# Kernel tuning notes

Measured on AMD Instinct MI355X. Metric: run time of the kernel, lower is better.

Reference implementation:

```python
import jax, jax.numpy as jnp
import numpy as np

B, L, D, H, PD = 4, 8192, 512, 8, 1
DK = D // H
EPS = 1e-5


def setup_inputs() -> dict:
    root = jax.random.key(0)
    ks = jax.random.split(root, 16)
    s = 0.02
    inp = {
        'query': jax.random.normal(ks[0], (B, L, D), jnp.float32),
        'key': jax.random.normal(ks[1], (B, L, D), jnp.float32),
        'value': jax.random.normal(ks[2], (B, L, D), jnp.float32),
        'pos': jax.random.uniform(ks[3], (B, L, PD), jnp.float32),
        # QKV projections (xavier-ish small + diagonal init, as in _reset_parameters)
        'Wq': s * jax.random.normal(ks[4], (D, D), jnp.float32) + 0.01 * jnp.eye(D),
        'bq': jnp.zeros((D,), jnp.float32),
        'Wk': s * jax.random.normal(ks[5], (D, D), jnp.float32) + 0.01 * jnp.eye(D),
        'bk': jnp.zeros((D,), jnp.float32),
        'Wv': s * jax.random.normal(ks[6], (D, D), jnp.float32) + 0.01 * jnp.eye(D),
        'bv': jnp.zeros((D,), jnp.float32),
        # per-head LayerNorm affine params for K and V: [H, DK]
        'gK': jnp.ones((H, DK), jnp.float32),
        'betaK': jnp.zeros((H, DK), jnp.float32),
        'gV': jnp.ones((H, DK), jnp.float32),
        'betaV': jnp.zeros((H, DK), jnp.float32),
        # output fc: (D + H*PD) -> D
        'fcW': s * jax.random.normal(ks[7], (D, D + H * PD), jnp.float32),
        'fcb': jnp.zeros((D,), jnp.float32),
    }
    return inp


def _proj(x, W, b):
    # [B,L,D] -> [B,H,L,DK]
    return (x @ W.T + b).reshape(B, L, H, DK).transpose(0, 2, 1, 3)


def _head_layernorm(x, g, b):
    # x: [B,H,L,DK]; per-head affine params g,b: [H,DK]; biased variance (torch LN)
    m = x.mean(-1, keepdims=True)
    v = x.var(-1, keepdims=True)
    xn = (x - m) * jax.lax.rsqrt(v + EPS)
    return xn * g[None, :, None, :] + b[None, :, None, :]


def reference(query, key, value, pos, Wq, bq, Wk, bk, Wv, bv,
              gK, betaK, gV, betaV, fcW, fcb):
    q = _proj(query, Wq, bq)
    k = _proj(key, Wk, bk)
    v = _proj(value, Wv, bv)
    k = _head_layernorm(k, gK, betaK)
    v = _head_layernorm(v, gV, betaV)
    # positional concat: pos [B,L,PD] -> [B,H,L,PD], concat on feature dim
    p = jnp.broadcast_to(pos[:, None, :, :], (B, H, L, PD))
    q = jnp.concatenate([p, q], axis=-1)  # [B,H,L,DK+PD]
    k = jnp.concatenate([p, k], axis=-1)
    v = jnp.concatenate([p, v], axis=-1)
    # Galerkin linear attention: (K^T V)/L then Q @ that
    attn = jnp.einsum('bhld,bhle->bhde', k, v) / L  # [B,H,DK+PD,DK+PD]
    out = jnp.einsum('bhld,bhde->bhle', q, attn)    # [B,H,L,DK+PD]
    out = out.transpose(0, 2, 1, 3).reshape(B, L, H * (DK + PD))
    att_output = out @ fcW.T + fcb  # [B,L,D]
    return (att_output, attn)
```

## Files before the change

kernel.cpp:

```cpp
#include <hip/hip_runtime.h>

typedef __attribute__((ext_vector_type(8))) short short8;
typedef __attribute__((ext_vector_type(4))) float f32x4;
typedef __attribute__((ext_vector_type(4))) unsigned short ushort4v;
typedef __attribute__((ext_vector_type(4))) unsigned int uint4v;
typedef unsigned short ushort;
typedef unsigned int uint;

#define B_  4
#define L_  8192
#define D_  512
#define H_  8
#define F_  65
#define CF_ 520
#define CFP_ 544
#define KVS_ 80
#define EPS_ 1e-5f

__device__ __forceinline__ ushort f2b(float f) {
    uint x = __float_as_uint(f);
    uint r = (x + 0x7FFFu + ((x >> 16) & 1u)) >> 16;
    return (ushort)r;
}
__device__ __forceinline__ float b2f(ushort u) {
    return __uint_as_float(((uint)u) << 16);
}

#define GLD16(gptr, sptr) \
    __builtin_amdgcn_global_load_lds((const __attribute__((address_space(1))) void*)(gptr), \
                                     (__attribute__((address_space(3))) void*)(sptr), 16, 0, 0)

__device__ __forceinline__ size_t pk_off(int col, int row) {
    return (size_t)(col >> 5) * 4096 + (size_t)(((col >> 3) & 3) * 1024 + row * 8 + (col & 7));
}

__global__ __launch_bounds__(256)
void cast_w(const float* __restrict__ Wq, const float* __restrict__ Wk,
            const float* __restrict__ Wv, ushort* __restrict__ Wb)
{
    const int g = blockIdx.x * 256 + threadIdx.x;
    const int inner = g & 511;
    const int tileIdx = g >> 9;
    const int w   = inner >> 7;
    const int row = inner & 127;
    const int ks  = tileIdx & 15;
    const int nt  = (tileIdx >> 4) & 3;
    const int z   = tileIdx >> 6;
    const float* __restrict__ src = (z == 0) ? Wq : (z == 1) ? Wk : Wv;
    const float* s = &src[(size_t)(nt * 128 + row) * D_ + ks * 32 + w * 8];
    const float4 f0 = *(const float4*)s;
    const float4 f1 = *(const float4*)(s + 4);
    short8 v;
    v[0] = (short)f2b(f0.x); v[1] = (short)f2b(f0.y);
    v[2] = (short)f2b(f0.z); v[3] = (short)f2b(f0.w);
    v[4] = (short)f2b(f1.x); v[5] = (short)f2b(f1.y);
    v[6] = (short)f2b(f1.z); v[7] = (short)f2b(f1.w);
    *(short8*)&Wb[(size_t)tileIdx * 4096 + inner * 8] = v;
}

__global__ __launch_bounds__(256, 2)
void proj_mfma(const float* __restrict__ Xq, const float* __restrict__ Xk,
               const float* __restrict__ Xv, const ushort* __restrict__ Wb,
               const float* __restrict__ bq, const float* __restrict__ bk,
               const float* __restrict__ bv, const float* __restrict__ pos,
               const float* __restrict__ gK, const float* __restrict__ betaK,
               const float* __restrict__ gV, const float* __restrict__ betaV,
               ushort* __restrict__ Qc, ushort* __restrict__ Kh,
               ushort* __restrict__ Vh)
{
    const int x  = blockIdx.x;
    const int m0 = (((x >> 4) << 3) + (x & 7)) * 128;
    const int nh = (x >> 3) & 1;
    const int n0 = nh * 256;
    const int z  = blockIdx.y;

    const float*  __restrict__ X    = (z == 0) ? Xq : (z == 1) ? Xk : Xv;
    const float*  __restrict__ bias = (z == 0) ? bq : (z == 1) ? bk : bv;

    const int t  = threadIdx.x;
    const int w  = t >> 6, l = t & 63;
    const int wm = (w >> 1) * 64, wn = (w & 1) * 128;
    const int lg = l >> 4, lm = l & 15;

    __shared__ __align__(16) float sAf[2][4096];
    __shared__ __align__(16) short sB[2][8192];

    f32x4 acc[4][8];
#pragma unroll
    for (int i = 0; i < 4; ++i)
#pragma unroll
        for (int j = 0; j < 8; ++j) acc[i][j] = (f32x4){0.f, 0.f, 0.f, 0.f};

    const int lr = l >> 3;
    const int hg = (l & 7) ^ lr;
    const float* ag[4]; int alo[4];
#pragma unroll
    for (int i = 0; i < 4; ++i) {
        const int row = (w * 4 + i) * 8 + lr;
        ag[i]  = &X[(size_t)(m0 + row) * D_ + hg * 4];
        alo[i] = (w * 4 + i) * 256;
    }

    const ushort* bsrc0 = Wb + (size_t)((z * 4 + nh * 2) * 16) * 4096 + w * 1024 + l * 8;
    const ushort* bsrc1 = bsrc0 + (size_t)16 * 4096;
    const int blo0 = w * 1024, blo1 = w * 1024 + 512;

    int a0o[4], a1o[4], bro[8];
#pragma unroll
    for (int i = 0; i < 4; ++i) {
        const int r = wm + i * 16 + lm;
        a0o[i] = r * 32 + (((lg * 2)     ^ (r & 7)) * 4);
        a1o[i] = r * 32 + (((lg * 2 + 1) ^ (r & 7)) * 4);
    }
#pragma unroll
    for (int i = 0; i < 8; ++i) {
        const int col = wn + i * 16 + lm;
        bro[i] = (col >> 7) * 4096 + lg * 1024 + (col & 127) * 8;
    }

    auto stage = [&](int ks, int buf) {
#pragma unroll
        for (int i = 0; i < 4; ++i) GLD16(ag[i] + ks * 32, &sAf[buf][alo[i]]);
        GLD16(bsrc0 + (size_t)ks * 4096,       &sB[buf][blo0]);
        GLD16(bsrc0 + (size_t)ks * 4096 + 512, &sB[buf][blo1]);
        GLD16(bsrc1 + (size_t)ks * 4096,       &sB[buf][4096 + blo0]);
        GLD16(bsrc1 + (size_t)ks * 4096 + 512, &sB[buf][4096 + blo1]);
    };

    stage(0, 0);
    int cur = 0;
#pragma unroll
    for (int ks = 0; ks < 16; ++ks) {
        __syncthreads();
        if (ks < 15) stage(ks + 1, cur ^ 1);

        short8 af[4], bfv[8];
#pragma unroll
        for (int i = 0; i < 4; ++i) {
            const f32x4 A0 = *(const f32x4*)&sAf[cur][a0o[i]];
            const f32x4 A1 = *(const f32x4*)&sAf[cur][a1o[i]];
            uint u0, u1, u2, u3;
            asm("v_cvt_pk_bf16_f32 %0, %1, %2" : "=v"(u0) : "v"(A0[0]), "v"(A0[1]));
            asm("v_cvt_pk_bf16_f32 %0, %1, %2" : "=v"(u1) : "v"(A0[2]), "v"(A0[3]));
            asm("v_cvt_pk_bf16_f32 %0, %1, %2" : "=v"(u2) : "v"(A1[0]), "v"(A1[1]));
            asm("v_cvt_pk_bf16_f32 %0, %1, %2" : "=v"(u3) : "v"(A1[2]), "v"(A1[3]));
            union { uint4v u4; short8 s8; } cv;
            cv.u4 = (uint4v){u0, u1, u2, u3};
            af[i] = cv.s8;
        }
#pragma unroll
        for (int i = 0; i < 8; ++i) bfv[i] = *(const short8*)&sB[cur][bro[i]];
#pragma unroll
        for (int mt = 0; mt < 4; ++mt)
#pragma unroll
            for (int nt = 0; nt < 8; ++nt)
                acc[mt][nt] = __builtin_amdgcn_mfma_f32_16x16x32_bf16(
                    af[mt], bfv[nt], acc[mt][nt], 0, 0, 0);

        cur ^= 1;
    }

    const int h0 = (n0 + wn) >> 6;
    float bvv[8];
#pragma unroll
    for (int nt = 0; nt < 8; ++nt) bvv[nt] = bias[n0 + wn + nt * 16 + lm];

    if (z == 0) {
#pragma unroll
        for (int mt = 0; mt < 4; ++mt) {
#pragma unroll
            for (int r = 0; r < 4; ++r) {
                const int m = m0 + wm + mt * 16 + lg * 4 + r;
                const int mtile = m >> 7, rowin = m & 127;
                ushort* tb = Qc + (size_t)(mtile * 17) * 4096 + rowin * 8;
#pragma unroll
                for (int nt = 0; nt < 8; ++nt) {
                    const int col = (h0 + (nt >> 2)) * F_ + 1 + (nt & 3) * 16 + lm;
                    tb[pk_off(col, 0)] = f2b(acc[mt][nt][r] + bvv[nt]);
                }
                if (lm == 15) {
                    tb[pk_off(h0 * F_, 0)]       = f2b(pos[m]);
                    tb[pk_off((h0 + 1) * F_, 0)] = f2b(pos[m]);
                }
                if (h0 == 6 && lm < 12) {
                    const int wreg = 1 + (lm >> 2);
                    const int e2 = (lm & 3) * 2;
                    *(uint*)&tb[(size_t)16 * 4096 + wreg * 1024 + e2] = 0u;
                }
            }
        }
    } else {
        const float* gp = (z == 1) ? gK : gV;
        const float* bp = (z == 1) ? betaK : betaV;
        ushort* Oh = (z == 1) ? Kh : Vh;
        float gg[8], bb2[8];
#pragma unroll
        for (int nt = 0; nt < 8; ++nt) {
            const int idx = (h0 + (nt >> 2)) * 64 + (nt & 3) * 16 + lm;
            gg[nt]  = gp[idx];
            bb2[nt] = bp[idx];
        }
#pragma unroll
        for (int mt = 0; mt < 4; ++mt) {
#pragma unroll
            for (int r = 0; r < 4; ++r) {
                const int m = m0 + wm + mt * 16 + lg * 4 + r;
                const int bb = m >> 13, ll = m & 8191;
#pragma unroll
                for (int g = 0; g < 2; ++g) {
                    const float v0 = acc[mt][g * 4 + 0][r] + bvv[g * 4 + 0];
                    const float v1 = acc[mt][g * 4 + 1][r] + bvv[g * 4 + 1];
                    const float v2 = acc[mt][g * 4 + 2][r] + bvv[g * 4 + 2];
                    const float v3 = acc[mt][g * 4 + 3][r] + bvv[g * 4 + 3];
                    float s = v0 + v1 + v2 + v3;
                    float q = v0 * v0 + v1 * v1 + v2 * v2 + v3 * v3;
                    s += __shfl_xor(s, 1); s += __shfl_xor(s, 2);
                    s += __shfl_xor(s, 4); s += __shfl_xor(s, 8);
                    q += __shfl_xor(q, 1); q += __shfl_xor(q, 2);
                    q += __shfl_xor(q, 4); q += __shfl_xor(q, 8);
                    const float mean = s * (1.f / 64.f);
                    const float var = q * (1.f / 64.f) - mean * mean;
                    const float rs = rsqrtf(var + EPS_);
                    const int h = h0 + g;
                    ushort* row = Oh + ((size_t)(bb * H_ + h) * L_ + ll) * KVS_;
                    row[1 + 0 * 16 + lm] = f2b((v0 - mean) * rs * gg[g * 4 + 0] + bb2[g * 4 + 0]);
                    row[1 + 1 * 16 + lm] = f2b((v1 - mean) * rs * gg[g * 4 + 1] + bb2[g * 4 + 1]);
                    row[1 + 2 * 16 + lm] = f2b((v2 - mean) * rs * gg[g * 4 + 2] + bb2[g * 4 + 2]);
                    row[1 + 3 * 16 + lm] = f2b((v3 - mean) * rs * gg[g * 4 + 3] + bb2[g * 4 + 3]);
                    if (lm == 15) row[0] = f2b(pos[m]);
                    else          row[F_ + lm] = 0;
                }
            }
        }
    }
}

__global__ __launch_bounds__(256)
void attn_accum(const ushort* __restrict__ Kh, const ushort* __restrict__ Vh,
                float* __restrict__ attn_acc)
{
    const int s = blockIdx.x;
    const int h = blockIdx.y;
    const int b = blockIdx.z;
    const int t = threadIdx.x;

    __shared__ __align__(16) float Ks[64][84];
    __shared__ __align__(16) float Vs[64][84];

    const size_t base = ((size_t)(b * H_ + h) * L_ + s * 512) * KVS_;

    float acc[5][5];
#pragma unroll
    for (int i = 0; i < 5; ++i)
#pragma unroll
        for (int j = 0; j < 5; ++j) acc[i][j] = 0.f;

    const int dg = t / 13, eg = t % 13;
    const bool act = (t < 169);
    const int d0 = dg * 5, e0 = eg * 5;

    for (int c = 0; c < 8; ++c) {
#pragma unroll
        for (int i = 0; i < 3; ++i) {
            const int slot = t + i * 256;
            if (slot < 640) {
                const int r = slot / 10;
                const int cc = (slot - r * 10) * 8;
                const size_t g = base + (size_t)(c * 64 + r) * KVS_ + cc;
                const short8 kv = *(const short8*)(const void*)&Kh[g];
                const short8 vv = *(const short8*)(const void*)&Vh[g];
                float* kd = &Ks[r][cc];
                float* vd = &Vs[r][cc];
#pragma unroll
                for (int e = 0; e < 8; ++e) {
                    kd[e] = b2f((ushort)kv[e]);
                    vd[e] = b2f((ushort)vv[e]);
                }
            }
        }
        __syncthreads();
        if (act) {
#pragma unroll 2
            for (int l = 0; l < 64; ++l) {
                float kf[5], vf[5];
#pragma unroll
                for (int i = 0; i < 5; ++i) kf[i] = Ks[l][d0 + i];
#pragma unroll
                for (int j = 0; j < 5; ++j) vf[j] = Vs[l][e0 + j];
#pragma unroll
                for (int i = 0; i < 5; ++i)
#pragma unroll
                    for (int j = 0; j < 5; ++j)
                        acc[i][j] = fmaf(kf[i], vf[j], acc[i][j]);
            }
        }
        __syncthreads();
    }

    if (act) {
        float* dst = attn_acc + (size_t)(b * H_ + h) * (F_ * F_);
#pragma unroll
        for (int i = 0; i < 5; ++i)
#pragma unroll
            for (int j = 0; j < 5; ++j)
                atomicAdd(&dst[(d0 + i) * F_ + (e0 + j)], acc[i][j]);
    }
}

__global__ __launch_bounds__(256)
void attn_fin_G(const float* __restrict__ attn_acc, const float* __restrict__ fcW,
                float* __restrict__ attn_out, ushort* __restrict__ Gt)
{
    const int nc = blockIdx.x;
    const int h = blockIdx.y;
    const int b = blockIdx.z;
    const int t = threadIdx.x;

    __shared__ float S[F_][F_];
    __shared__ float Wl[64][F_];

    const float inv = 1.0f / (float)L_;
    const float* __restrict__ src = attn_acc + (size_t)(b * H_ + h) * F_ * F_;
    for (int idx = t; idx < F_ * F_; idx += 256) {
        const float v = src[idx] * inv;
        S[idx / F_][idx % F_] = v;
        if (nc == 0) attn_out[(size_t)(b * H_ + h) * F_ * F_ + idx] = v;
    }
    for (int idx = t; idx < 64 * F_; idx += 256) {
        const int j = idx / F_;
        const int e = idx - j * F_;
        Wl[j][e] = fcW[(size_t)(nc * 64 + j) * CF_ + h * F_ + e];
    }
    __syncthreads();

    for (int idx = t; idx < F_ * 64; idx += 256) {
        const int d = idx >> 6;
        const int j = idx & 63;
        float g = 0.f;
#pragma unroll 5
        for (int e = 0; e < F_; ++e) g = fmaf(S[d][e], Wl[j][e], g);
        const int jg = nc * 64 + j;
        const int col = h * F_ + d;
        Gt[(size_t)((b * 4 + (jg >> 7)) * 17) * 4096 + (jg & 127) * 8 + pk_off(col, 0)] = f2b(g);
    }
    if (h == 7) {
        for (int i2 = t; i2 < 64 * 24; i2 += 256) {
            const int j = i2 / 24;
            const int col = CF_ + (i2 % 24);
            const int jg = nc * 64 + j;
            Gt[(size_t)((b * 4 + (jg >> 7)) * 17) * 4096 + (jg & 127) * 8 + pk_off(col, 0)] = 0;
        }
    }
}

__global__ __launch_bounds__(256, 2)
void out_mfma(const ushort* __restrict__ Qc, const ushort* __restrict__ Gt,
              const float* __restrict__ fcb, float* __restrict__ out)
{
    const int x  = blockIdx.x;
    const int m0 = (((x >> 4) << 3) + (x & 7)) * 128;
    const int nh = (x >> 3) & 1;
    const int n0 = nh * 256;
    const int b  = blockIdx.z;
    const int t  = threadIdx.x;
    const int w  = t >> 6, l = t & 63;
    const int wm = (w >> 1) * 64, wn = (w & 1) * 128;
    const int lg = l >> 4, lm = l & 15;

    __shared__ __align__(16) short sA[2][4096];
    __shared__ __align__(16) short sB[2][8192];

    f32x4 acc[4][8];
#pragma unroll
    for (int i = 0; i < 4; ++i)
#pragma unroll
        for (int j = 0; j < 8; ++j) acc[i][j] = (f32x4){0.f, 0.f, 0.f, 0.f};

    const int mtA = (b * L_ + m0) >> 7;
    const ushort* asrc  = Qc + (size_t)(mtA * 17) * 4096 + w * 1024 + l * 8;
    const ushort* bsrc0 = Gt + (size_t)((b * 4 + nh * 2) * 17) * 4096 + w * 1024 + l * 8;
    const ushort* bsrc1 = bsrc0 + (size_t)17 * 4096;
    const int lo0 = w * 1024, lo1 = w * 1024 + 512;

    int aro[4], bro[8];
#pragma unroll
    for (int i = 0; i < 4; ++i)
        aro[i] = lg * 1024 + (wm + i * 16 + lm) * 8;
#pragma unroll
    for (int i = 0; i < 8; ++i) {
        const int col = wn + i * 16 + lm;
        bro[i] = (col >> 7) * 4096 + lg * 1024 + (col & 127) * 8;
    }

    auto stage = [&](int ks, int buf) {
        GLD16(asrc  + (size_t)ks * 4096,       &sA[buf][lo0]);
        GLD16(asrc  + (size_t)ks * 4096 + 512, &sA[buf][lo1]);
        GLD16(bsrc0 + (size_t)ks * 4096,       &sB[buf][lo0]);
        GLD16(bsrc0 + (size_t)ks * 4096 + 512, &sB[buf][lo1]);
        GLD16(bsrc1 + (size_t)ks * 4096,       &sB[buf][4096 + lo0]);
        GLD16(bsrc1 + (size_t)ks * 4096 + 512, &sB[buf][4096 + lo1]);
    };

    stage(0, 0);
    int cur = 0;
#pragma unroll
    for (int ks = 0; ks < 17; ++ks) {
        __syncthreads();
        if (ks < 16) stage(ks + 1, cur ^ 1);

        short8 af[4], bfv[8];
#pragma unroll
        for (int i = 0; i < 4; ++i) af[i]  = *(const short8*)&sA[cur][aro[i]];
#pragma unroll
        for (int i = 0; i < 8; ++i) bfv[i] = *(const short8*)&sB[cur][bro[i]];
#pragma unroll
        for (int mt = 0; mt < 4; ++mt)
#pragma unroll
            for (int nt = 0; nt < 8; ++nt)
                acc[mt][nt] = __builtin_amdgcn_mfma_f32_16x16x32_bf16(
                    af[mt], bfv[nt], acc[mt][nt], 0, 0, 0);

        cur ^= 1;
    }

    float bvv[8];
#pragma unroll
    for (int nt = 0; nt < 8; ++nt) bvv[nt] = fcb[n0 + wn + nt * 16 + lm];

#pragma unroll
    for (int mt = 0; mt < 4; ++mt) {
#pragma unroll
        for (int r = 0; r < 4; ++r) {
            const int row = m0 + wm + mt * 16 + lg * 4 + r;
            float* orow = out + ((size_t)b * L_ + row) * D_;
#pragma unroll
            for (int nt = 0; nt < 8; ++nt)
                orow[n0 + wn + nt * 16 + lm] = acc[mt][nt][r] + bvv[nt];
        }
    }
}

extern "C" void kernel_launch(void* const* d_in, const int* in_sizes, int n_in,
                              void* d_out, int out_size, void* d_ws, size_t ws_size,
                              hipStream_t stream)
{
    const float* query = (const float*)d_in[0];
    const float* key   = (const float*)d_in[1];
    const float* value = (const float*)d_in[2];
    const float* pos   = (const float*)d_in[3];
    const float* Wq    = (const float*)d_in[4];
    const float* bq    = (const float*)d_in[5];
    const float* Wk    = (const float*)d_in[6];
    const float* bk    = (const float*)d_in[7];
    const float* Wv    = (const float*)d_in[8];
    const float* bv    = (const float*)d_in[9];
    const float* gK    = (const float*)d_in[10];
    const float* betaK = (const float*)d_in[11];
    const float* gV    = (const float*)d_in[12];
    const float* betaV = (const float*)d_in[13];
    const float* fcW   = (const float*)d_in[14];
    const float* fcb   = (const float*)d_in[15];

    char* ws = (char*)d_ws;
    ushort* Qc       = (ushort*)(ws + 0);
    ushort* Kh       = (ushort*)(ws + 35651584);
    ushort* Vh       = (ushort*)(ws + 77594624);
    ushort* Wb       = (ushort*)(ws + 119537664);
    float*  attn_acc = (float*) (ws + 121110528);
    ushort* Gt       = (ushort*)(ws + 121651328);

    float* att_out  = (float*)d_out;
    float* attn_out = att_out + 16777216;

    hipMemsetAsync(attn_acc, 0, (size_t)135200 * sizeof(float), stream);

    cast_w<<<dim3(384), 256, 0, stream>>>(Wq, Wk, Wv, Wb);

    proj_mfma<<<dim3(512, 3), 256, 0, stream>>>(
        query, key, value, Wb, bq, bk, bv, pos,
        gK, betaK, gV, betaV, Qc, Kh, Vh);

    attn_accum<<<dim3(16, 8, 4), 256, 0, stream>>>(Kh, Vh, attn_acc);

    attn_fin_G<<<dim3(8, 8, 4), 256, 0, stream>>>(attn_acc, fcW, attn_out, Gt);

    out_mfma<<<dim3(128, 1, 4), 256, 0, stream>>>(Qc, Gt, fcb, att_out);
}
```

Baseline: 460.3 us.

## Fold Q projection into per-batch output weight, skip Q materialization

```diff
diff --git a/kernel.cpp b/kernel.cpp
--- a/kernel.cpp
+++ b/kernel.cpp
@@ -2,7 +2,6 @@
 
 typedef __attribute__((ext_vector_type(8))) short short8;
 typedef __attribute__((ext_vector_type(4))) float f32x4;
-typedef __attribute__((ext_vector_type(4))) unsigned short ushort4v;
 typedef __attribute__((ext_vector_type(4))) unsigned int uint4v;
 typedef unsigned short ushort;
 typedef unsigned int uint;
@@ -12,8 +11,6 @@
 #define D_  512
 #define H_  8
 #define F_  65
-#define CF_ 520
-#define CFP_ 544
 #define KVS_ 80
 #define EPS_ 1e-5f
 
@@ -30,13 +27,10 @@
     __builtin_amdgcn_global_load_lds((const __attribute__((address_space(1))) void*)(gptr), \
                                      (__attribute__((address_space(3))) void*)(sptr), 16, 0, 0)
 
-__device__ __forceinline__ size_t pk_off(int col, int row) {
-    return (size_t)(col >> 5) * 4096 + (size_t)(((col >> 3) & 3) * 1024 + row * 8 + (col & 7));
-}
 
 __global__ __launch_bounds__(256)
-void cast_w(const float* __restrict__ Wq, const float* __restrict__ Wk,
-            const float* __restrict__ Wv, ushort* __restrict__ Wb)
+void cast_w(const float* __restrict__ Wk, const float* __restrict__ Wv,
+            ushort* __restrict__ Wb)
 {
     const int g = blockIdx.x * 256 + threadIdx.x;
     const int inner = g & 511;
@@ -46,7 +40,7 @@
     const int ks  = tileIdx & 15;
     const int nt  = (tileIdx >> 4) & 3;
     const int z   = tileIdx >> 6;
-    const float* __restrict__ src = (z == 0) ? Wq : (z == 1) ? Wk : Wv;
+    const float* __restrict__ src = (z == 0) ? Wk : Wv;
     const float* s = &src[(size_t)(nt * 128 + row) * D_ + ks * 32 + w * 8];
     const float4 f0 = *(const float4*)s;
     const float4 f1 = *(const float4*)(s + 4);
@@ -58,32 +52,29 @@
     *(short8*)&Wb[(size_t)tileIdx * 4096 + inner * 8] = v;
 }
 
-__global__ __launch_bounds__(256, 2)
-void proj_mfma(const float* __restrict__ Xq, const float* __restrict__ Xk,
-               const float* __restrict__ Xv, const ushort* __restrict__ Wb,
-               const float* __restrict__ bq, const float* __restrict__ bk,
-               const float* __restrict__ bv, const float* __restrict__ pos,
+__global__ __launch_bounds__(512, 2)
+void proj_mfma(const float* __restrict__ Xk, const float* __restrict__ Xv,
+               const ushort* __restrict__ Wb,
+               const float* __restrict__ bk, const float* __restrict__ bv,
+               const float* __restrict__ pos,
                const float* __restrict__ gK, const float* __restrict__ betaK,
                const float* __restrict__ gV, const float* __restrict__ betaV,
-               ushort* __restrict__ Qc, ushort* __restrict__ Kh,
-               ushort* __restrict__ Vh)
+               ushort* __restrict__ Kh, ushort* __restrict__ Vh)
 {
     const int x  = blockIdx.x;
-    const int m0 = (((x >> 4) << 3) + (x & 7)) * 128;
-    const int nh = (x >> 3) & 1;
-    const int n0 = nh * 256;
+    const int m0 = ((x & 7) * 32 + (x >> 3)) * 128;
     const int z  = blockIdx.y;
 
-    const float*  __restrict__ X    = (z == 0) ? Xq : (z == 1) ? Xk : Xv;
-    const float*  __restrict__ bias = (z == 0) ? bq : (z == 1) ? bk : bv;
+    const float* __restrict__ X    = (z == 0) ? Xk : Xv;
+    const float* __restrict__ bias = (z == 0) ? bk : bv;
 
     const int t  = threadIdx.x;
     const int w  = t >> 6, l = t & 63;
-    const int wm = (w >> 1) * 64, wn = (w & 1) * 128;
+    const int wm = (w >> 2) * 64, wn = (w & 3) * 128;
     const int lg = l >> 4, lm = l & 15;
 
     __shared__ __align__(16) float sAf[2][4096];
-    __shared__ __align__(16) short sB[2][8192];
+    __shared__ __align__(16) short sB[2][16384];
 
     f32x4 acc[4][8];
 #pragma unroll
@@ -93,17 +84,18 @@
 
     const int lr = l >> 3;
     const int hg = (l & 7) ^ lr;
-    const float* ag[4]; int alo[4];
-#pragma unroll
-    for (int i = 0; i < 4; ++i) {
-        const int row = (w * 4 + i) * 8 + lr;
+    const float* ag[2]; int alo[2];
+#pragma unroll
+    for (int i = 0; i < 2; ++i) {
+        const int row = w * 16 + i * 8 + lr;
         ag[i]  = &X[(size_t)(m0 + row) * D_ + hg * 4];
-        alo[i] = (w * 4 + i) * 256;
-    }
-
-    const ushort* bsrc0 = Wb + (size_t)((z * 4 + nh * 2) * 16) * 4096 + w * 1024 + l * 8;
-    const ushort* bsrc1 = bsrc0 + (size_t)16 * 4096;
-    const int blo0 = w * 1024, blo1 = w * 1024 + 512;
+        alo[i] = (w * 2 + i) * 256;
+    }
+
+    const ushort* bsrc[4];
+#pragma unroll
+    for (int nt = 0; nt < 4; ++nt)
+        bsrc[nt] = Wb + (size_t)((z * 4 + nt) * 16) * 4096 + t * 8;
 
     int a0o[4], a1o[4], bro[8];
 #pragma unroll
@@ -120,11 +112,10 @@
 
     auto stage = [&](int ks, int buf) {
 #pragma unroll
-        for (int i = 0; i < 4; ++i) GLD16(ag[i] + ks * 32, &sAf[buf][alo[i]]);
-        GLD16(bsrc0 + (size_t)ks * 4096,       &sB[buf][blo0]);
-        GLD16(bsrc0 + (size_t)ks * 4096 + 512, &sB[buf][blo1]);
-        GLD16(bsrc1 + (size_t)ks * 4096,       &sB[buf][4096 + blo0]);
-        GLD16(bsrc1 + (size_t)ks * 4096 + 512, &sB[buf][4096 + blo1]);
+        for (int i = 0; i < 2; ++i) GLD16(ag[i] + ks * 32, &sAf[buf][alo[i]]);
+#pragma unroll
+        for (int nt = 0; nt < 4; ++nt)
+            GLD16(bsrc[nt] + (size_t)ks * 4096, &sB[buf][nt * 4096 + t * 8]);
     };
 
     stage(0, 0);
@@ -160,76 +151,50 @@
         cur ^= 1;
     }
 
-    const int h0 = (n0 + wn) >> 6;
+    const int h0 = wn >> 6;
     float bvv[8];
 #pragma unroll
-    for (int nt = 0; nt < 8; ++nt) bvv[nt] = bias[n0 + wn + nt * 16 + lm];
-
-    if (z == 0) {
-#pragma unroll
-        for (int mt = 0; mt < 4; ++mt) {
-#pragma unroll
-            for (int r = 0; r < 4; ++r) {
-                const int m = m0 + wm + mt * 16 + lg * 4 + r;
-                const int mtile = m >> 7, rowin = m & 127;
-                ushort* tb = Qc + (size_t)(mtile * 17) * 4096 + rowin * 8;
-#pragma unroll
-                for (int nt = 0; nt < 8; ++nt) {
-                    const int col = (h0 + (nt >> 2)) * F_ + 1 + (nt & 3) * 16 + lm;
-                    tb[pk_off(col, 0)] = f2b(acc[mt][nt][r] + bvv[nt]);
-                }
-                if (lm == 15) {
-                    tb[pk_off(h0 * F_, 0)]       = f2b(pos[m]);
-                    tb[pk_off((h0 + 1) * F_, 0)] = f2b(pos[m]);
-                }
-                if (h0 == 6 && lm < 12) {
-                    const int wreg = 1 + (lm >> 2);
-                    const int e2 = (lm & 3) * 2;
-                    *(uint*)&tb[(size_t)16 * 4096 + wreg * 1024 + e2] = 0u;
-                }
-            }
-        }
-    } else {
-        const float* gp = (z == 1) ? gK : gV;
-        const float* bp = (z == 1) ? betaK : betaV;
-        ushort* Oh = (z == 1) ? Kh : Vh;
-        float gg[8], bb2[8];
-#pragma unroll
-        for (int nt = 0; nt < 8; ++nt) {
-            const int idx = (h0 + (nt >> 2)) * 64 + (nt & 3) * 16 + lm;
-            gg[nt]  = gp[idx];
-            bb2[nt] = bp[idx];
-        }
-#pragma unroll
-        for (int mt = 0; mt < 4; ++mt) {
-#pragma unroll
-            for (int r = 0; r < 4; ++r) {
-                const int m = m0 + wm + mt * 16 + lg * 4 + r;
-                const int bb = m >> 13, ll = m & 8191;
-#pragma unroll
-                for (int g = 0; g < 2; ++g) {
-                    const float v0 = acc[mt][g * 4 + 0][r] + bvv[g * 4 + 0];
-                    const float v1 = acc[mt][g * 4 + 1][r] + bvv[g * 4 + 1];
-                    const float v2 = acc[mt][g * 4 + 2][r] + bvv[g * 4 + 2];
-                    const float v3 = acc[mt][g * 4 + 3][r] + bvv[g * 4 + 3];
-                    float s = v0 + v1 + v2 + v3;
-                    float q = v0 * v0 + v1 * v1 + v2 * v2 + v3 * v3;
-                    s += __shfl_xor(s, 1); s += __shfl_xor(s, 2);
-                    s += __shfl_xor(s, 4); s += __shfl_xor(s, 8);
-                    q += __shfl_xor(q, 1); q += __shfl_xor(q, 2);
-                    q += __shfl_xor(q, 4); q += __shfl_xor(q, 8);
-                    const float mean = s * (1.f / 64.f);
-                    const float var = q * (1.f / 64.f) - mean * mean;
-                    const float rs = rsqrtf(var + EPS_);
-                    const int h = h0 + g;
-                    ushort* row = Oh + ((size_t)(bb * H_ + h) * L_ + ll) * KVS_;
-                    row[1 + 0 * 16 + lm] = f2b((v0 - mean) * rs * gg[g * 4 + 0] + bb2[g * 4 + 0]);
-                    row[1 + 1 * 16 + lm] = f2b((v1 - mean) * rs * gg[g * 4 + 1] + bb2[g * 4 + 1]);
-                    row[1 + 2 * 16 + lm] = f2b((v2 - mean) * rs * gg[g * 4 + 2] + bb2[g * 4 + 2]);
-                    row[1 + 3 * 16 + lm] = f2b((v3 - mean) * rs * gg[g * 4 + 3] + bb2[g * 4 + 3]);
-                    if (lm == 15) row[0] = f2b(pos[m]);
-                    else          row[F_ + lm] = 0;
-                }
+    for (int nt = 0; nt < 8; ++nt) bvv[nt] = bias[wn + nt * 16 + lm];
+
+    const float* gp = (z == 0) ? gK : gV;
+    const float* bp = (z == 0) ? betaK : betaV;
+    ushort* Oh = (z == 0) ? Kh : Vh;
+    float gg[8], bb2[8];
+#pragma unroll
+    for (int nt = 0; nt < 8; ++nt) {
+        const int idx = (h0 + (nt >> 2)) * 64 + (nt & 3) * 16 + lm;
+        gg[nt]  = gp[idx];
+        bb2[nt] = bp[idx];
+    }
+#pragma unroll
+    for (int mt = 0; mt < 4; ++mt) {
+#pragma unroll
+        for (int r = 0; r < 4; ++r) {
+            const int m = m0 + wm + mt * 16 + lg * 4 + r;
+            const int bb = m >> 13, ll = m & 8191;
+#pragma unroll
+            for (int g = 0; g < 2; ++g) {
+                const float v0 = acc[mt][g * 4 + 0][r] + bvv[g * 4 + 0];
+                const float v1 = acc[mt][g * 4 + 1][r] + bvv[g * 4 + 1];
+                const float v2 = acc[mt][g * 4 + 2][r] + bvv[g * 4 + 2];
+                const float v3 = acc[mt][g * 4 + 3][r] + bvv[g * 4 + 3];
+                float s = v0 + v1 + v2 + v3;
+                float q = v0 * v0 + v1 * v1 + v2 * v2 + v3 * v3;
+                s += __shfl_xor(s, 1); s += __shfl_xor(s, 2);
+                s += __shfl_xor(s, 4); s += __shfl_xor(s, 8);
+                q += __shfl_xor(q, 1); q += __shfl_xor(q, 2);
+                q += __shfl_xor(q, 4); q += __shfl_xor(q, 8);
+                const float mean = s * (1.f / 64.f);
+                const float var = q * (1.f / 64.f) - mean * mean;
+                const float rs = rsqrtf(var + EPS_);
+                const int h = h0 + g;
+                ushort* row = Oh + ((size_t)(bb * H_ + h) * L_ + ll) * KVS_;
+                row[1 + 0 * 16 + lm] = f2b((v0 - mean) * rs * gg[g * 4 + 0] + bb2[g * 4 + 0]);
+                row[1 + 1 * 16 + lm] = f2b((v1 - mean) * rs * gg[g * 4 + 1] + bb2[g * 4 + 1]);
+                row[1 + 2 * 16 + lm] = f2b((v2 - mean) * rs * gg[g * 4 + 2] + bb2[g * 4 + 2]);
+                row[1 + 3 * 16 + lm] = f2b((v3 - mean) * rs * gg[g * 4 + 3] + bb2[g * 4 + 3]);
+                if (lm == 15) row[0] = f2b(pos[m]);
+                else          row[F_ + lm] = 0;
             }
         }
     }
@@ -308,8 +273,9 @@
 }
 
 __global__ __launch_bounds__(256)
-void attn_fin_G(const float* __restrict__ attn_acc, const float* __restrict__ fcW,
-                float* __restrict__ attn_out, ushort* __restrict__ Gt)
+void attn_fin(const float* __restrict__ attn_acc, const float* __restrict__ fcW,
+              float* __restrict__ attn_out, float* __restrict__ Gq,
+              float* __restrict__ gt0)
 {
     const int nc = blockIdx.x;
     const int h = blockIdx.y;
@@ -329,7 +295,7 @@
     for (int idx = t; idx < 64 * F_; idx += 256) {
         const int j = idx / F_;
         const int e = idx - j * F_;
-        Wl[j][e] = fcW[(size_t)(nc * 64 + j) * CF_ + h * F_ + e];
+        Wl[j][e] = fcW[(size_t)(nc * 64 + j) * (H_ * F_) + h * F_ + e];
     }
     __syncthreads();
 
@@ -339,36 +305,107 @@
         float g = 0.f;
 #pragma unroll 5
         for (int e = 0; e < F_; ++e) g = fmaf(S[d][e], Wl[j][e], g);
-        const int jg = nc * 64 + j;
-        const int col = h * F_ + d;
-        Gt[(size_t)((b * 4 + (jg >> 7)) * 17) * 4096 + (jg & 127) * 8 + pk_off(col, 0)] = f2b(g);
-    }
-    if (h == 7) {
-        for (int i2 = t; i2 < 64 * 24; i2 += 256) {
-            const int j = i2 / 24;
-            const int col = CF_ + (i2 % 24);
-            const int jg = nc * 64 + j;
-            Gt[(size_t)((b * 4 + (jg >> 7)) * 17) * 4096 + (jg & 127) * 8 + pk_off(col, 0)] = 0;
-        }
-    }
-}
-
-__global__ __launch_bounds__(256, 2)
-void out_mfma(const ushort* __restrict__ Qc, const ushort* __restrict__ Gt,
-              const float* __restrict__ fcb, float* __restrict__ out)
+        const int n = nc * 64 + j;
+        if (d == 0) gt0[((size_t)b * 512 + n) * 8 + h] = g;
+        else        Gq[((size_t)b * 512 + n) * 512 + h * 64 + (d - 1)] = g;
+    }
+}
+
+__global__ __launch_bounds__(256)
+void w2_build(const float* __restrict__ Gq, const float* __restrict__ gt0,
+              const float* __restrict__ Wq, const float* __restrict__ bq,
+              const float* __restrict__ fcb, ushort* __restrict__ W2pk,
+              float* __restrict__ Pv, float* __restrict__ C2v)
+{
+    const int kt  = blockIdx.x;
+    const int ntb = blockIdx.y;
+    const int b   = blockIdx.z;
+    const int t   = threadIdx.x;
+    const int n0 = ntb * 64, k0 = kt * 64;
+
+    __shared__ float Sg[64][65];
+    __shared__ float Sw[64][65];
+
+    const float* __restrict__ gq = Gq + (size_t)b * 262144;
+
+    float acc[4][4];
+#pragma unroll
+    for (int i = 0; i < 4; ++i)
+#pragma unroll
+        for (int j = 0; j < 4; ++j) acc[i][j] = 0.f;
+    float c2a[4] = {0.f, 0.f, 0.f, 0.f};
+
+    const int tn = t >> 4, tk = t & 15;
+
+    for (int dc = 0; dc < 8; ++dc) {
+        const int d0 = dc * 64;
+        for (int idx = t; idx < 4096; idx += 256) {
+            const int rr = idx >> 6, cc = idx & 63;
+            Sg[rr][cc] = gq[(size_t)(n0 + rr) * 512 + d0 + cc];
+            Sw[rr][cc] = Wq[(size_t)(d0 + rr) * 512 + k0 + cc];
+        }
+        __syncthreads();
+        for (int dd = 0; dd < 64; ++dd) {
+            float gf[4], wf[4];
+#pragma unroll
+            for (int i = 0; i < 4; ++i) gf[i] = Sg[tn * 4 + i][dd];
+#pragma unroll
+            for (int j = 0; j < 4; ++j) wf[j] = Sw[dd][tk * 4 + j];
+#pragma unroll
+            for (int i = 0; i < 4; ++i)
+#pragma unroll
+                for (int j = 0; j < 4; ++j)
+                    acc[i][j] = fmaf(gf[i], wf[j], acc[i][j]);
+        }
+        if (tk == 0) {
+            for (int dd = 0; dd < 64; ++dd) {
+                const float bqv = bq[d0 + dd];
+#pragma unroll
+                for (int i = 0; i < 4; ++i)
+                    c2a[i] = fmaf(bqv, Sg[tn * 4 + i][dd], c2a[i]);
+            }
+        }
+        __syncthreads();
+    }
+
+    ushort* wp = W2pk + (size_t)b * 262144;
+#pragma unroll
+    for (int i = 0; i < 4; ++i)
+#pragma unroll
+        for (int j = 0; j < 4; ++j) {
+            const int n = n0 + tn * 4 + i;
+            const int k = k0 + tk * 4 + j;
+            wp[(size_t)((n >> 7) * 16 + (k >> 5)) * 4096 +
+               ((k >> 3) & 3) * 1024 + (n & 127) * 8 + (k & 7)] = f2b(acc[i][j]);
+        }
+    if (kt == 0 && tk == 0) {
+#pragma unroll
+        for (int i = 0; i < 4; ++i) {
+            const int n = n0 + tn * 4 + i;
+            float p = 0.f;
+#pragma unroll
+            for (int h = 0; h < 8; ++h) p += gt0[((size_t)b * 512 + n) * 8 + h];
+            Pv[b * 512 + n]  = p;
+            C2v[b * 512 + n] = fcb[n] + c2a[i];
+        }
+    }
+}
+
+__global__ __launch_bounds__(512, 2)
+void out_mfma(const float* __restrict__ query, const ushort* __restrict__ W2pk,
+              const float* __restrict__ pos, const float* __restrict__ Pv,
+              const float* __restrict__ C2v, float* __restrict__ out)
 {
     const int x  = blockIdx.x;
-    const int m0 = (((x >> 4) << 3) + (x & 7)) * 128;
-    const int nh = (x >> 3) & 1;
-    const int n0 = nh * 256;
-    const int b  = blockIdx.z;
+    const int m0 = ((x & 7) * 32 + (x >> 3)) * 128;
+    const int b  = m0 >> 13;
     const int t  = threadIdx.x;
     const int w  = t >> 6, l = t & 63;
-    const int wm = (w >> 1) * 64, wn = (w & 1) * 128;
+    const int wm = (w >> 2) * 64, wn = (w & 3) * 128;
     const int lg = l >> 4, lm = l & 15;
 
-    __shared__ __align__(16) short sA[2][4096];
-    __shared__ __align__(16) short sB[2][8192];
+    __shared__ __align__(16) float sAf[2][4096];
+    __shared__ __align__(16) short sB[2][16384];
 
     f32x4 acc[4][8];
 #pragma unroll
@@ -376,16 +413,28 @@
 #pragma unroll
         for (int j = 0; j < 8; ++j) acc[i][j] = (f32x4){0.f, 0.f, 0.f, 0.f};
 
-    const int mtA = (b * L_ + m0) >> 7;
-    const ushort* asrc  = Qc + (size_t)(mtA * 17) * 4096 + w * 1024 + l * 8;
-    const ushort* bsrc0 = Gt + (size_t)((b * 4 + nh * 2) * 17) * 4096 + w * 1024 + l * 8;
-    const ushort* bsrc1 = bsrc0 + (size_t)17 * 4096;
-    const int lo0 = w * 1024, lo1 = w * 1024 + 512;
-
-    int aro[4], bro[8];
-#pragma unroll
-    for (int i = 0; i < 4; ++i)
-        aro[i] = lg * 1024 + (wm + i * 16 + lm) * 8;
+    const int lr = l >> 3;
+    const int hg = (l & 7) ^ lr;
+    const float* ag[2]; int alo[2];
+#pragma unroll
+    for (int i = 0; i < 2; ++i) {
+        const int row = w * 16 + i * 8 + lr;
+        ag[i]  = &query[(size_t)(m0 + row) * D_ + hg * 4];
+        alo[i] = (w * 2 + i) * 256;
+    }
+
+    const ushort* bsrc[4];
+#pragma unroll
+    for (int nt = 0; nt < 4; ++nt)
+        bsrc[nt] = W2pk + (size_t)b * 262144 + (size_t)(nt * 16) * 4096 + t * 8;
+
+    int a0o[4], a1o[4], bro[8];
+#pragma unroll
+    for (int i = 0; i < 4; ++i) {
+        const int r = wm + i * 16 + lm;
+        a0o[i] = r * 32 + (((lg * 2)     ^ (r & 7)) * 4);
+        a1o[i] = r * 32 + (((lg * 2 + 1) ^ (r & 7)) * 4);
+    }
 #pragma unroll
     for (int i = 0; i < 8; ++i) {
         const int col = wn + i * 16 + lm;
@@ -393,24 +442,34 @@
     }
 
     auto stage = [&](int ks, int buf) {
-        GLD16(asrc  + (size_t)ks * 4096,       &sA[buf][lo0]);
-        GLD16(asrc  + (size_t)ks * 4096 + 512, &sA[buf][lo1]);
-        GLD16(bsrc0 + (size_t)ks * 4096,       &sB[buf][lo0]);
-        GLD16(bsrc0 + (size_t)ks * 4096 + 512, &sB[buf][lo1]);
-        GLD16(bsrc1 + (size_t)ks * 4096,       &sB[buf][4096 + lo0]);
-        GLD16(bsrc1 + (size_t)ks * 4096 + 512, &sB[buf][4096 + lo1]);
+#pragma unroll
+        for (int i = 0; i < 2; ++i) GLD16(ag[i] + ks * 32, &sAf[buf][alo[i]]);
+#pragma unroll
+        for (int nt = 0; nt < 4; ++nt)
+            GLD16(bsrc[nt] + (size_t)ks * 4096, &sB[buf][nt * 4096 + t * 8]);
     };
 
     stage(0, 0);
     int cur = 0;
 #pragma unroll
-    for (int ks = 0; ks < 17; ++ks) {
+    for (int ks = 0; ks < 16; ++ks) {
         __syncthreads();
-        if (ks < 16) stage(ks + 1, cur ^ 1);
+        if (ks < 15) stage(ks + 1, cur ^ 1);
 
         short8 af[4], bfv[8];
 #pragma unroll
-        for (int i = 0; i < 4; ++i) af[i]  = *(const short8*)&sA[cur][aro[i]];
+        for (int i = 0; i < 4; ++i) {
+            const f32x4 A0 = *(const f32x4*)&sAf[cur][a0o[i]];
+            const f32x4 A1 = *(const f32x4*)&sAf[cur][a1o[i]];
+            uint u0, u1, u2, u3;
+            asm("v_cvt_pk_bf16_f32 %0, %1, %2" : "=v"(u0) : "v"(A0[0]), "v"(A0[1]));
+            asm("v_cvt_pk_bf16_f32 %0, %1, %2" : "=v"(u1) : "v"(A0[2]), "v"(A0[3]));
+            asm("v_cvt_pk_bf16_f32 %0, %1, %2" : "=v"(u2) : "v"(A1[0]), "v"(A1[1]));
+            asm("v_cvt_pk_bf16_f32 %0, %1, %2" : "=v"(u3) : "v"(A1[2]), "v"(A1[3]));
+            union { uint4v u4; short8 s8; } cv;
+            cv.u4 = (uint4v){u0, u1, u2, u3};
+            af[i] = cv.s8;
+        }
 #pragma unroll
         for (int i = 0; i < 8; ++i) bfv[i] = *(const short8*)&sB[cur][bro[i]];
 #pragma unroll
@@ -423,19 +482,24 @@
         cur ^= 1;
     }
 
-    float bvv[8];
-#pragma unroll
-    for (int nt = 0; nt < 8; ++nt) bvv[nt] = fcb[n0 + wn + nt * 16 + lm];
+    float pv[8], c2[8];
+#pragma unroll
+    for (int nt = 0; nt < 8; ++nt) {
+        const int n = wn + nt * 16 + lm;
+        pv[nt] = Pv[b * 512 + n];
+        c2[nt] = C2v[b * 512 + n];
+    }
 
 #pragma unroll
     for (int mt = 0; mt < 4; ++mt) {
 #pragma unroll
         for (int r = 0; r < 4; ++r) {
             const int row = m0 + wm + mt * 16 + lg * 4 + r;
-            float* orow = out + ((size_t)b * L_ + row) * D_;
+            const float pr = pos[row];
+            float* orow = out + (size_t)row * D_;
 #pragma unroll
             for (int nt = 0; nt < 8; ++nt)
-                orow[n0 + wn + nt * 16 + lm] = acc[mt][nt][r] + bvv[nt];
+                orow[wn + nt * 16 + lm] = acc[mt][nt][r] + pr * pv[nt] + c2[nt];
         }
     }
 }
@@ -462,27 +526,31 @@
     const float* fcb   = (const float*)d_in[15];
 
     char* ws = (char*)d_ws;
-    ushort* Qc       = (ushort*)(ws + 0);
-    ushort* Kh       = (ushort*)(ws + 35651584);
-    ushort* Vh       = (ushort*)(ws + 77594624);
-    ushort* Wb       = (ushort*)(ws + 119537664);
-    float*  attn_acc = (float*) (ws + 121110528);
-    ushort* Gt       = (ushort*)(ws + 121651328);
+    ushort* Kh       = (ushort*)(ws + 0);
+    ushort* Vh       = (ushort*)(ws + 41943040);
+    ushort* Wb       = (ushort*)(ws + 83886080);
+    float*  attn_acc = (float*) (ws + 84934656);
+    float*  Gq       = (float*) (ws + 85479424);
+    float*  gt0      = (float*) (ws + 89673728);
+    ushort* W2pk     = (ushort*)(ws + 89739264);
+    float*  Pv       = (float*) (ws + 91836416);
+    float*  C2v      = (float*) (ws + 91844608);
 
     float* att_out  = (float*)d_out;
     float* attn_out = att_out + 16777216;
 
     hipMemsetAsync(attn_acc, 0, (size_t)135200 * sizeof(float), stream);
 
-    cast_w<<<dim3(384), 256, 0, stream>>>(Wq, Wk, Wv, Wb);
-
-    proj_mfma<<<dim3(512, 3), 256, 0, stream>>>(
-        query, key, value, Wb, bq, bk, bv, pos,
-        gK, betaK, gV, betaV, Qc, Kh, Vh);
+    cast_w<<<dim3(256), 256, 0, stream>>>(Wk, Wv, Wb);
+
+    proj_mfma<<<dim3(256, 2), 512, 0, stream>>>(
+        key, value, Wb, bk, bv, pos, gK, betaK, gV, betaV, Kh, Vh);
 
     attn_accum<<<dim3(16, 8, 4), 256, 0, stream>>>(Kh, Vh, attn_acc);
 
-    attn_fin_G<<<dim3(8, 8, 4), 256, 0, stream>>>(attn_acc, fcW, attn_out, Gt);
-
-    out_mfma<<<dim3(128, 1, 4), 256, 0, stream>>>(Qc, Gt, fcb, att_out);
-}
+    attn_fin<<<dim3(8, 8, 4), 256, 0, stream>>>(attn_acc, fcW, attn_out, Gq, gt0);
+
+    w2_build<<<dim3(8, 8, 4), 256, 0, stream>>>(Gq, gt0, Wq, bq, fcb, W2pk, Pv, C2v);
+
+    out_mfma<<<dim3(256), 512, 0, stream>>>(query, W2pk, pos, Pv, C2v, att_out);
+}
```

Result: slower. 480.8 us (+4.5%).
